# Performance work log

Hardware: AMD Instinct MI355X
Metric: run time of the kernel (lower is better)

The kernel has to match this reference:

```python
import jax, jax.numpy as jnp
import numpy as np


def setup_inputs() -> dict:
    key = jax.random.key(0)
    ks = jax.random.split(key, 7)
    Bsz, Dm, L, N = 2, 1536, 2048, 16
    x = jax.random.normal(ks[0], (Bsz, Dm, L), jnp.float32)
    delta = jax.random.uniform(ks[1], (Bsz, Dm, L), jnp.float32, 1e-3, 0.1)  # positive step sizes
    A = -jax.random.uniform(ks[2], (Dm, N), jnp.float32, 0.5, 1.5)  # negative real A for stability
    B = jax.random.normal(ks[3], (Bsz, N, L), jnp.float32)
    C = jax.random.normal(ks[4], (Bsz, N, L), jnp.float32)
    D = jax.random.normal(ks[5], (Dm,), jnp.float32)
    z = jax.random.normal(ks[6], (Bsz, Dm, L), jnp.float32)
    return {"x": x, "delta": delta, "A": A, "B": B, "C": C, "D": D, "z": z}


def reference(x, delta, A, B, C, D, z):
    # x, delta, z: [b, d, l]; A: [d, n]; B, C: [b, n, l]; D: [d]
    dtype_in = x.dtype
    x = x.astype(jnp.float32)
    delta = delta.astype(jnp.float32)
    Bm = B.astype(jnp.float32)
    Cm = C.astype(jnp.float32)

    # time-major for scan: [l, b, ...]
    dl = jnp.moveaxis(delta, 2, 0)   # l b d
    xl = jnp.moveaxis(x, 2, 0)       # l b d
    Bl = jnp.moveaxis(Bm, 2, 0)      # l b n
    Cl = jnp.moveaxis(Cm, 2, 0)      # l b n

    h0 = jnp.zeros((x.shape[0], A.shape[0], A.shape[1]), jnp.float32)  # b d n

    def step(h, inp):
        d_t, x_t, B_t, C_t = inp
        deltaA = jnp.exp(d_t[:, :, None] * A[None, :, :])      # exp(einsum('bdl,dn->bdln')) at token t
        deltaB = d_t[:, :, None] * B_t[:, None, :]              # einsum('bdl,bnl->bdln') at token t
        h = deltaA * h + deltaB * x_t[:, :, None]               # Hx update
        y = jnp.einsum('bdn,bn->bd', h, C_t)                    # Yh readout
        return h, y

    _, ys = jax.lax.scan(step, h0, (dl, xl, Bl, Cl))            # ys: [l, b, d]
    y = jnp.moveaxis(ys, 0, 2)                                  # b d l

    out = y + x * D[None, :, None]
    out = out * jax.nn.silu(z)
    return out.astype(dtype_in)
```

## Files before the change

kernel.cpp:

```cpp
#include <hip/hip_runtime.h>

#define LOG2E 1.44269504088896340736f
#define DM 1536
#define LL  2048
#define NN  16
#define NCH 64
#define CL  32

__device__ __forceinline__ float fexp2(float v){ return __builtin_amdgcn_exp2f(v); }
__device__ __forceinline__ float frcp(float v){ return __builtin_amdgcn_rcpf(v); }

__device__ __forceinline__ void load16(const float* __restrict__ p, float* v){
    const float4 a=*(const float4*)p,     b=*(const float4*)(p+4),
                 c=*(const float4*)(p+8), d=*(const float4*)(p+12);
    v[0]=a.x; v[1]=a.y; v[2]=a.z; v[3]=a.w;
    v[4]=b.x; v[5]=b.y; v[6]=b.z; v[7]=b.w;
    v[8]=c.x; v[9]=c.y; v[10]=c.z; v[11]=c.w;
    v[12]=d.x; v[13]=d.y; v[14]=d.z; v[15]=d.w;
}

__global__ __launch_bounds__(256) void transpose_bc(
        const float* __restrict__ Bm, const float* __restrict__ Cm,
        float* __restrict__ Bt, float* __restrict__ Ct){
    int o = blockIdx.x*256 + threadIdx.x;
    int n = o & 15, c = (o>>4) & 63, r = (o>>10) & 31, b = o>>15;
    int i = (b*NN + n)*LL + c*CL + r;
    Bt[o] = Bm[i];
    Ct[o] = Cm[i];
}

__global__ __launch_bounds__(256, 2) void ssm_scan(
    const float* __restrict__ x, const float* __restrict__ delta,
    const float* __restrict__ A, const float* __restrict__ Dv,
    const float* __restrict__ z, const float* __restrict__ Bt,
    const float* __restrict__ Ct, float* __restrict__ out)
{
    __shared__ float sd[4][CL*64];
    __shared__ float sx[4][CL*64];

    const int lane = threadIdx.x & 63;
    const int w    = threadIdx.x >> 6;
    const int row  = blockIdx.x*4 + w;
    const int b    = (row >= DM) ? 1 : 0;
    const int d    = row - b*DM;

    float* sdw = sd[w];
    float* sxw = sx[w];

    const long base = (long)row*LL;
    const float* gd = delta + base;
    const float* gx = x + base;

    for (int k = 0; k < LL; k += 256){
        const int t0 = k + lane*4;
        const float4 dv = *(const float4*)(gd + t0);
        const float4 xv = *(const float4*)(gx + t0);
        const float dd[4]={dv.x,dv.y,dv.z,dv.w};
        const float xx[4]={xv.x,xv.y,xv.z,xv.w};
#pragma unroll
        for (int j=0;j<4;++j){
            const int t = t0 + j;
            const int r = t & 31, c = t >> 5;
            const int a = r*64 + (c ^ r);
            sdw[a] = dd[j];
            sxw[a] = xx[j];
        }
    }

    float A2[NN];
#pragma unroll
    for (int n=0;n<NN;++n) A2[n] = A[d*NN+n] * LOG2E;

    const float* bq = Bt + (long)b*(CL*NCH*NN) + lane*NN;
    const float* cq = Ct + (long)b*(CL*NCH*NN) + lane*NN;

    float G[NN];
#pragma unroll
    for (int n=0;n<NN;++n) G[n] = 0.f;
    float dsum = 0.f;
#pragma unroll 2
    for (int r=0;r<CL;++r){
        const int a = r*64 + (lane ^ r);
        const float d_r = sdw[a];
        const float x_r = sxw[a];
        float bb[16];
        load16(bq + r*(NCH*NN), bb);
        dsum += d_r;
        const float dx = d_r * x_r;
#pragma unroll
        for (int n=0;n<NN;++n){
            const float e = fexp2(d_r*A2[n]);
            G[n] = __builtin_fmaf(e, G[n], bb[n]*dx);
        }
    }
    float P[NN];
#pragma unroll
    for (int n=0;n<NN;++n) P[n] = fexp2(dsum*A2[n]);

#pragma unroll
    for (int s=1;s<64;s<<=1){
#pragma unroll
        for (int n=0;n<NN;++n){
            const float pl = __shfl_up(P[n], s);
            const float gl = __shfl_up(G[n], s);
            if (lane >= s){
                G[n] = __builtin_fmaf(P[n], gl, G[n]);
                P[n] *= pl;
            }
        }
    }
    float h[NN];
#pragma unroll
    for (int n=0;n<NN;++n){
        const float gp = __shfl_up(G[n], 1);
        h[n] = (lane==0) ? 0.f : gp;
    }

    const float Dd = Dv[d];
#pragma unroll 2
    for (int r=0;r<CL;++r){
        const int a = r*64 + (lane ^ r);
        const float d_r = sdw[a];
        const float x_r = sxw[a];
        float bb[16], cc[16];
        load16(bq + r*(NCH*NN), bb);
        load16(cq + r*(NCH*NN), cc);
        const float dx = d_r * x_r;
        float y0=0.f, y1=0.f, y2=0.f, y3=0.f;
#pragma unroll
        for (int n=0;n<NN;n+=4){
            const float e0=fexp2(d_r*A2[n+0]);
            h[n+0]=__builtin_fmaf(e0,h[n+0],bb[n+0]*dx); y0=__builtin_fmaf(h[n+0],cc[n+0],y0);
            const float e1=fexp2(d_r*A2[n+1]);
            h[n+1]=__builtin_fmaf(e1,h[n+1],bb[n+1]*dx); y1=__builtin_fmaf(h[n+1],cc[n+1],y1);
            const float e2=fexp2(d_r*A2[n+2]);
            h[n+2]=__builtin_fmaf(e2,h[n+2],bb[n+2]*dx); y2=__builtin_fmaf(h[n+2],cc[n+2],y2);
            const float e3=fexp2(d_r*A2[n+3]);
            h[n+3]=__builtin_fmaf(e3,h[n+3],bb[n+3]*dx); y3=__builtin_fmaf(h[n+3],cc[n+3],y3);
        }
        const float y = (y0+y1)+(y2+y3);
        sxw[a] = __builtin_fmaf(x_r, Dd, y);
    }

    const float* gz = z + base;
    float* go = out + base;
    for (int k=0;k<LL;k+=256){
        const int t0 = k + lane*4;
        const float4 zv = *(const float4*)(gz + t0);
        const float zz[4]={zv.x,zv.y,zv.z,zv.w};
        float o[4];
#pragma unroll
        for (int j=0;j<4;++j){
            const int t = t0 + j;
            const int r = t & 31, c = t >> 5;
            const float yd = sxw[r*64 + (c ^ r)];
            const float sig = frcp(1.f + fexp2(-zz[j]*LOG2E));
            o[j] = yd * (zz[j]*sig);
        }
        float4 o4 = {o[0],o[1],o[2],o[3]};
        *(float4*)(go + t0) = o4;
    }
}

extern "C" void kernel_launch(void* const* d_in, const int* in_sizes, int n_in,
                              void* d_out, int out_size, void* d_ws, size_t ws_size,
                              hipStream_t stream) {
    const float* x     = (const float*)d_in[0];
    const float* delta = (const float*)d_in[1];
    const float* A     = (const float*)d_in[2];
    const float* B     = (const float*)d_in[3];
    const float* C     = (const float*)d_in[4];
    const float* Dv    = (const float*)d_in[5];
    const float* z     = (const float*)d_in[6];
    float* out = (float*)d_out;

    float* Bt = (float*)d_ws;
    float* Ct = Bt + 2*LL*NN;

    transpose_bc<<<dim3(256), dim3(256), 0, stream>>>(B, C, Bt, Ct);
    ssm_scan<<<dim3((2*DM)/4), dim3(256), 0, stream>>>(x, delta, A, Dv, z, Bt, Ct, out);
}
```

Measured before the change: 183.5 us.

## Pack delta and x as fp16 in LDS, prefetch B/C, raise occupancy

Stores delta and x as a packed fp16 pair in one shared-memory word, halving LDS use per block so three blocks can fit per CU (launch bounds raised to 3). B and C loads are software-pipelined one timestep ahead in both scan passes. The B/C transpose kernel now reads float4 and uses fewer blocks. The trade-off is reduced precision for delta and x inside the scan, plus extra register pressure from the prefetch buffers.

```diff
diff --git a/kernel.cpp b/kernel.cpp
--- a/kernel.cpp
+++ b/kernel.cpp
@@ -1,4 +1,5 @@
 #include <hip/hip_runtime.h>
+#include <hip/hip_fp16.h>
 
 #define LOG2E 1.44269504088896340736f
 #define DM 1536
@@ -19,39 +20,57 @@
     v[12]=d.x; v[13]=d.y; v[14]=d.z; v[15]=d.w;
 }
 
+__device__ __forceinline__ float packdx(float d, float x){
+    unsigned u = (unsigned)__half_as_ushort(__float2half_rn(d))
+               | ((unsigned)__half_as_ushort(__float2half_rn(x)) << 16);
+    return __uint_as_float(u);
+}
+__device__ __forceinline__ void unpackdx(float f, float& d, float& x){
+    const unsigned u = __float_as_uint(f);
+    d = __half2float(__ushort_as_half((unsigned short)(u & 0xffffu)));
+    x = __half2float(__ushort_as_half((unsigned short)(u >> 16)));
+}
+
 __global__ __launch_bounds__(256) void transpose_bc(
         const float* __restrict__ Bm, const float* __restrict__ Cm,
         float* __restrict__ Bt, float* __restrict__ Ct){
-    int o = blockIdx.x*256 + threadIdx.x;
-    int n = o & 15, c = (o>>4) & 63, r = (o>>10) & 31, b = o>>15;
-    int i = (b*NN + n)*LL + c*CL + r;
-    Bt[o] = Bm[i];
-    Ct[o] = Cm[i];
-}
-
-__global__ __launch_bounds__(256, 2) void ssm_scan(
+    const int q  = blockIdx.x*256 + threadIdx.x;
+    const int t0 = (q & 511) << 2;
+    const int n  = (q >> 9) & 15;
+    const int b  = q >> 13;
+    const long i = (long)(b*NN + n)*LL + t0;
+    const float4 bv = *(const float4*)(Bm + i);
+    const float4 cv = *(const float4*)(Cm + i);
+    const float bb[4]={bv.x,bv.y,bv.z,bv.w}, cc[4]={cv.x,cv.y,cv.z,cv.w};
+#pragma unroll
+    for (int j=0;j<4;++j){
+        const int t = t0 + j;
+        const int o = ((b*CL + (t&31))*NCH + (t>>5))*NN + n;
+        Bt[o] = bb[j];
+        Ct[o] = cc[j];
+    }
+}
+
+__global__ __launch_bounds__(256, 3) void ssm_scan(
     const float* __restrict__ x, const float* __restrict__ delta,
     const float* __restrict__ A, const float* __restrict__ Dv,
     const float* __restrict__ z, const float* __restrict__ Bt,
     const float* __restrict__ Ct, float* __restrict__ out)
 {
-    __shared__ float sd[4][CL*64];
-    __shared__ float sx[4][CL*64];
+    __shared__ float sdx[4][CL*64];
 
     const int lane = threadIdx.x & 63;
     const int w    = threadIdx.x >> 6;
     const int row  = blockIdx.x*4 + w;
     const int b    = (row >= DM) ? 1 : 0;
     const int d    = row - b*DM;
-
-    float* sdw = sd[w];
-    float* sxw = sx[w];
+    float* sw = sdx[w];
 
     const long base = (long)row*LL;
     const float* gd = delta + base;
     const float* gx = x + base;
 
-    for (int k = 0; k < LL; k += 256){
+    for (int k=0;k<LL;k+=256){
         const int t0 = k + lane*4;
         const float4 dv = *(const float4*)(gd + t0);
         const float4 xv = *(const float4*)(gx + t0);
@@ -59,11 +78,8 @@
         const float xx[4]={xv.x,xv.y,xv.z,xv.w};
 #pragma unroll
         for (int j=0;j<4;++j){
-            const int t = t0 + j;
-            const int r = t & 31, c = t >> 5;
-            const int a = r*64 + (c ^ r);
-            sdw[a] = dd[j];
-            sxw[a] = xx[j];
+            const int t = t0 + j, r = t & 31, c = t >> 5;
+            sw[r*64 + (c^r)] = packdx(dd[j], xx[j]);
         }
     }
 
@@ -78,19 +94,24 @@
 #pragma unroll
     for (int n=0;n<NN;++n) G[n] = 0.f;
     float dsum = 0.f;
+    float bb[NN];
+    load16(bq, bb);
 #pragma unroll 2
     for (int r=0;r<CL;++r){
-        const int a = r*64 + (lane ^ r);
-        const float d_r = sdw[a];
-        const float x_r = sxw[a];
-        float bb[16];
-        load16(bq + r*(NCH*NN), bb);
+        float nb[NN];
+        if (r+1 < CL) load16(bq + (r+1)*(NCH*NN), nb);
+        float d_r, x_r;
+        unpackdx(sw[r*64 + (lane^r)], d_r, x_r);
         dsum += d_r;
         const float dx = d_r * x_r;
 #pragma unroll
         for (int n=0;n<NN;++n){
             const float e = fexp2(d_r*A2[n]);
             G[n] = __builtin_fmaf(e, G[n], bb[n]*dx);
+        }
+        if (r+1 < CL){
+#pragma unroll
+            for (int n=0;n<NN;++n) bb[n] = nb[n];
         }
     }
     float P[NN];
@@ -117,14 +138,19 @@
     }
 
     const float Dd = Dv[d];
+    float cc[NN];
+    load16(bq, bb);
+    load16(cq, cc);
 #pragma unroll 2
     for (int r=0;r<CL;++r){
+        float nb[NN], nc[NN];
+        if (r+1 < CL){
+            load16(bq + (r+1)*(NCH*NN), nb);
+            load16(cq + (r+1)*(NCH*NN), nc);
+        }
         const int a = r*64 + (lane ^ r);
-        const float d_r = sdw[a];
-        const float x_r = sxw[a];
-        float bb[16], cc[16];
-        load16(bq + r*(NCH*NN), bb);
-        load16(cq + r*(NCH*NN), cc);
+        float d_r, x_r;
+        unpackdx(sw[a], d_r, x_r);
         const float dx = d_r * x_r;
         float y0=0.f, y1=0.f, y2=0.f, y3=0.f;
 #pragma unroll
@@ -139,7 +165,11 @@
             h[n+3]=__builtin_fmaf(e3,h[n+3],bb[n+3]*dx); y3=__builtin_fmaf(h[n+3],cc[n+3],y3);
         }
         const float y = (y0+y1)+(y2+y3);
-        sxw[a] = __builtin_fmaf(x_r, Dd, y);
+        sw[a] = __builtin_fmaf(x_r, Dd, y);
+        if (r+1 < CL){
+#pragma unroll
+            for (int n=0;n<NN;++n){ bb[n]=nb[n]; cc[n]=nc[n]; }
+        }
     }
 
     const float* gz = z + base;
@@ -151,9 +181,8 @@
         float o[4];
 #pragma unroll
         for (int j=0;j<4;++j){
-            const int t = t0 + j;
-            const int r = t & 31, c = t >> 5;
-            const float yd = sxw[r*64 + (c ^ r)];
+            const int t = t0 + j, r = t & 31, c = t >> 5;
+            const float yd = sw[r*64 + (c^r)];
             const float sig = frcp(1.f + fexp2(-zz[j]*LOG2E));
             o[j] = yd * (zz[j]*sig);
         }
@@ -177,6 +206,6 @@
     float* Bt = (float*)d_ws;
     float* Ct = Bt + 2*LL*NN;
 
-    transpose_bc<<<dim3(256), dim3(256), 0, stream>>>(B, C, Bt, Ct);
+    transpose_bc<<<dim3(64), dim3(256), 0, stream>>>(B, C, Bt, Ct);
     ssm_scan<<<dim3((2*DM)/4), dim3(256), 0, stream>>>(x, delta, A, Dv, z, Bt, Ct, out);
 }
```

Measured after the change: 185.2 us. About the same (+0.9%).
